# Kernel optimization log

Measured on AMD Instinct MI355X. Metric: run time of the kernel, lower is better.

The kernel has to match this reference:

```python
import math
import jax, jax.numpy as jnp
from jax import lax
import numpy as np

SIGMA_SCALES = [0.6 * 2 ** i for i in range(6)]  # [0.6, 1.2, 2.4, 4.8, 9.6, 19.2]


def _gauss1d(sigma: float, ks: int) -> np.ndarray:
    # ax = arange(-ks//2+1, ks//2+1) for odd ks == arange(ks) - ks//2 (symmetric)
    ax = np.arange(ks, dtype=np.float32) - ks // 2
    k = np.exp(-(ax ** 2) / (2.0 * sigma ** 2))
    return (k / k.sum()).astype(np.float32)


def _kernel_size(sigma: float) -> int:
    return max(7, 2 * math.ceil(3.0 * sigma) + 1)


def _gaussian_blur(img, sigma):
    # Separable depthwise Gaussian: the torch module's 2D kernel
    # exp(-(x^2+y^2)/2s^2)/Z factors exactly into outer(g1, g1) of normalized 1D kernels.
    B, C, H, W = img.shape
    ks = _kernel_size(sigma)
    p = ks // 2
    g1 = jnp.asarray(_gauss1d(sigma, ks), dtype=img.dtype)
    x = jnp.pad(img, ((0, 0), (0, 0), (p, p), (p, p)), mode='reflect')
    kh = jnp.broadcast_to(g1.reshape(1, 1, ks, 1), (C, 1, ks, 1))
    kw = jnp.broadcast_to(g1.reshape(1, 1, 1, ks), (C, 1, 1, ks))
    dn = ('NCHW', 'OIHW', 'NCHW')
    x = lax.conv_general_dilated(x, kh, (1, 1), 'VALID', dimension_numbers=dn,
                                 feature_group_count=C)
    x = lax.conv_general_dilated(x, kw, (1, 1), 'VALID', dimension_numbers=dn,
                                 feature_group_count=C)
    return x  # (B, C, H, W)


def setup_inputs() -> dict:
    key = jax.random.key(0)
    img = jax.random.normal(key, (8, 3, 512, 512), dtype=jnp.float32)
    return {"img": img}


def reference(img) -> jnp.ndarray:
    # gaussians = [img, G(s0)*img, G(s1)*img, ...]; each scale filters the ORIGINAL img.
    gaussians = [img]
    for sigma in SIGMA_SCALES:
        gaussians.append(_gaussian_blur(img, sigma))
    n = len(gaussians)
    subbands = [gaussians[i + 1] - gaussians[i] for i in range(n - 1)]
    subbands.append(gaussians[-1])
    return jnp.stack(subbands, axis=1)  # (B, len(scales)+1, C, H, W)
```

## Files before the change

### kernel.cpp

```cpp
#include <hip/hip_runtime.h>
#include <cmath>
#include <cstddef>

#define BATCH 8
#define CH    3
#define HH    512
#define WW    512
#define NSLOT 7
#define HWX   (HH*WW)

__device__ __host__ __forceinline__ int refl(int i, int n) {
    i = i < 0 ? -i : i;
    return i >= n ? 2 * n - 2 - i : i;
}

constexpr double cexp_(double x) {
    double r = x / 64.0, term = 1.0, s = 1.0;
    for (int i = 1; i < 26; ++i) { term *= r / i; s += term; }
    for (int j = 0; j < 6; ++j) s *= s;
    return s;
}

template<int KS> struct WArr { float w[KS + 16]; };

template<int KS>
constexpr WArr<KS> make_w(double sg) {
    WArr<KS> a{};
    double tmp[KS] = {};
    double sum = 0.0;
    for (int t = 0; t < KS; ++t) {
        const double ax = (double)(t - KS / 2);
        tmp[t] = cexp_(-(ax * ax) / (2.0 * sg * sg));
        sum += tmp[t];
    }
    for (int i = 0; i < KS + 16; ++i) a.w[i] = 0.0f;
    for (int t = 0; t < KS; ++t) a.w[8 + t] = (float)(tmp[t] / sum);
    return a;
}

__device__ constexpr WArr<7>   CW0 = make_w<7>(0.6);
__device__ constexpr WArr<9>   CW1 = make_w<9>(1.2);
__device__ constexpr WArr<17>  CW2 = make_w<17>(2.4);
__device__ constexpr WArr<31>  CW3 = make_w<31>(4.8);
__device__ constexpr WArr<59>  CW4 = make_w<59>(9.6);
__device__ constexpr WArr<117> CW5 = make_w<117>(19.2);

template<int KS> struct VWArr {
    static constexpr int TPAD = (KS + 30) & ~15;
    float w[TPAD + 16];
};

template<int KS>
constexpr VWArr<KS> make_vw(double sg) {
    VWArr<KS> a{};
    double tmp[KS] = {};
    double sum = 0.0;
    for (int t = 0; t < KS; ++t) {
        const double ax = (double)(t - KS / 2);
        tmp[t] = cexp_(-(ax * ax) / (2.0 * sg * sg));
        sum += tmp[t];
    }
    for (int i = 0; i < VWArr<KS>::TPAD + 16; ++i) a.w[i] = 0.0f;
    for (int t = 0; t < KS; ++t) a.w[16 + t] = (float)(tmp[t] / sum);
    return a;
}

__device__ constexpr VWArr<7>   VW0 = make_vw<7>(0.6);
__device__ constexpr VWArr<9>   VW1 = make_vw<9>(1.2);
__device__ constexpr VWArr<17>  VW2 = make_vw<17>(2.4);
__device__ constexpr VWArr<31>  VW3 = make_vw<31>(4.8);
__device__ constexpr VWArr<59>  VW4 = make_vw<59>(9.6);
__device__ constexpr VWArr<117> VW5 = make_vw<117>(19.2);

template<int KS, int PD>
__device__ __forceinline__ void vpass16(const float4* __restrict__ img4,
                                        float4* __restrict__ dst,
                                        int xt, int y0, const float* __restrict__ vw)
{
    constexpr int TPAD = (KS + 30) & ~15;
    float4 acc[16];
#pragma unroll
    for (int j = 0; j < 16; ++j) acc[j] = make_float4(0.f, 0.f, 0.f, 0.f);

    float ww[16];
#pragma unroll
    for (int m = 0; m < 16; ++m) ww[m] = vw[m];

#pragma unroll 1
    for (int tb = 0; tb < TPAD; tb += 16) {
        float wn[16];
#pragma unroll
        for (int k = 0; k < 16; ++k) wn[k] = vw[tb + 16 + k];
#pragma unroll
        for (int k = 0; k < 16; ++k) {
            const int yi = refl(y0 - PD + tb + k, HH);
            const float4 v = img4[(size_t)yi * (WW / 4) + xt];
#pragma unroll
            for (int j = 0; j < 16; ++j) {
                const int mi = 16 + k - j;
                const float wt = (mi < 16) ? ww[mi] : wn[mi - 16];
                acc[j].x = fmaf(wt, v.x, acc[j].x);
                acc[j].y = fmaf(wt, v.y, acc[j].y);
                acc[j].z = fmaf(wt, v.z, acc[j].z);
                acc[j].w = fmaf(wt, v.w, acc[j].w);
            }
        }
#pragma unroll
        for (int m = 0; m < 16; ++m) ww[m] = wn[m];
    }
#pragma unroll
    for (int j = 0; j < 16; ++j) dst[(size_t)(y0 + j) * (WW / 4) + xt] = acc[j];
}

__global__ __launch_bounds__(128) void vpass6_kernel(const float* __restrict__ img,
                                                     float* __restrict__ out)
{
    const int s  = blockIdx.x;
    const int xt = threadIdx.x;
    const int y0 = blockIdx.y * 16;
    const int bc = blockIdx.z;
    const int b = bc / CH, c = bc - b * CH;
    const float4* img4 = (const float4*)img + (size_t)bc * (HWX / 4);
    float4* dst = (float4*)out + ((size_t)((b * NSLOT + s + 1) * CH) + c) * (HWX / 4);
    switch (s) {
        case 0: vpass16<  7,  3>(img4, dst, xt, y0, VW0.w); break;
        case 1: vpass16<  9,  4>(img4, dst, xt, y0, VW1.w); break;
        case 2: vpass16< 17,  8>(img4, dst, xt, y0, VW2.w); break;
        case 3: vpass16< 31, 15>(img4, dst, xt, y0, VW3.w); break;
        case 4: vpass16< 59, 29>(img4, dst, xt, y0, VW4.w); break;
        default:vpass16<117, 58>(img4, dst, xt, y0, VW5.w); break;
    }
}

template<int KS>
__device__ __forceinline__ float4 hblur4c(const float* __restrict__ lrow, int xt,
                                          const WArr<KS>& W)
{
    constexpr int NT = (KS + 3) & ~3;
    const float4* l4 = (const float4*)lrow;
    float cb[16];
    {
        float4 t0 = l4[xt + 0];
        cb[0] = t0.x; cb[1] = t0.y; cb[2] = t0.z; cb[3] = t0.w;
        float4 t1 = l4[xt + 1];
        cb[4] = t1.x; cb[5] = t1.y; cb[6] = t1.z; cb[7] = t1.w;
    }
    float a[4] = {0.f, 0.f, 0.f, 0.f};
#pragma unroll
    for (int tb = 0; tb < NT; tb += 4) {
        const int ls = ((tb >> 2) + 2) & 3;
        float4 tn = l4[xt + (tb >> 2) + 2];
        cb[ls * 4 + 0] = tn.x; cb[ls * 4 + 1] = tn.y;
        cb[ls * 4 + 2] = tn.z; cb[ls * 4 + 3] = tn.w;
#pragma unroll
        for (int tt = 0; tt < 4; ++tt) {
            const float wt = W.w[8 + tb + tt];
#pragma unroll
            for (int j = 0; j < 4; ++j) {
                const int q    = tt + j;
                const int slot = ((tb >> 2) + (q >> 2)) & 3;
                a[j] = fmaf(wt, cb[slot * 4 + (q & 3)], a[j]);
            }
        }
    }
    return make_float4(a[0], a[1], a[2], a[3]);
}

#define LDSROW 3348

template<int OFF, int LEN, int PD>
__device__ __forceinline__ void stage_row(float* __restrict__ L,
                                          const float* __restrict__ g, int xt)
{
    const float4 v = ((const float4*)g)[xt];
    if constexpr ((PD & 3) == 0) {
        ((float4*)(L + OFF + PD))[xt] = v;
    } else {
        float* d = L + OFF + PD + 4 * xt;
        d[0] = v.x; d[1] = v.y; d[2] = v.z; d[3] = v.w;
    }
    if (xt < PD) L[OFF + xt] = g[PD - xt];
    for (int i = PD + 512 + xt; i < LEN; i += 128)
        L[OFF + i] = g[2 * WW - 2 - (i - PD)];
}

__device__ __forceinline__ float4 f4sub(float4 a, float4 b) {
    return make_float4(a.x - b.x, a.y - b.y, a.z - b.z, a.w - b.w);
}

__global__ __launch_bounds__(256) void hdiff6_kernel(const float* __restrict__ img,
                                                     float* __restrict__ out)
{
    __shared__ __align__(16) float lds[2][LDSROW];
    const int xt = threadIdx.x;
    const int r  = threadIdx.y;
    const int y  = blockIdx.y * 2 + r;
    const int bc = blockIdx.z;
    const int b = bc / CH, c = bc - b * CH;
    float* L = lds[r];

    const size_t rowoff = (size_t)y * WW;
    constexpr size_t SSTR = (size_t)CH * HWX;
    const float* g1 = out + ((size_t)((b * NSLOT + 1) * CH) + c) * HWX + rowoff;
    stage_row<   0, 524,  3>(L, g1,            xt);
    stage_row< 524, 528,  4>(L, g1 + 1 * SSTR, xt);
    stage_row<1052, 536,  8>(L, g1 + 2 * SSTR, xt);
    stage_row<1588, 548, 15>(L, g1 + 3 * SSTR, xt);
    stage_row<2136, 576, 29>(L, g1 + 4 * SSTR, xt);
    stage_row<2712, 636, 58>(L, g1 + 5 * SSTR, xt);
    __syncthreads();

    float4* out4 = (float4*)out;
    const size_t pbase = (size_t)y * (WW / 4) + xt;
#define OSL(s) (out4 + ((size_t)((b * NSLOT + (s)) * CH) + c) * (HWX / 4) + pbase)

    float4 gp = ((const float4*)(img + (size_t)bc * HWX + rowoff))[xt];
    float4 g;
    g = hblur4c<  7>(L +    0, xt, CW0); *OSL(0) = f4sub(g, gp); gp = g;
    g = hblur4c<  9>(L +  524, xt, CW1); *OSL(1) = f4sub(g, gp); gp = g;
    g = hblur4c< 17>(L + 1052, xt, CW2); *OSL(2) = f4sub(g, gp); gp = g;
    g = hblur4c< 31>(L + 1588, xt, CW3); *OSL(3) = f4sub(g, gp); gp = g;
    g = hblur4c< 59>(L + 2136, xt, CW4); *OSL(4) = f4sub(g, gp); gp = g;
    g = hblur4c<117>(L + 2712, xt, CW5); *OSL(5) = f4sub(g, gp);
    *OSL(6) = g;
#undef OSL
}

extern "C" void kernel_launch(void* const* d_in, const int* in_sizes, int n_in,
                              void* d_out, int out_size, void* d_ws, size_t ws_size,
                              hipStream_t stream) {
    const float* img = (const float*)d_in[0];
    float* out = (float*)d_out;

    const dim3 bv(128, 1), gv(6, HH / 16, BATCH * CH);
    hipLaunchKernelGGL(vpass6_kernel, gv, bv, 0, stream, img, out);

    const dim3 bh(128, 2), gh(1, HH / 2, BATCH * CH);
    hipLaunchKernelGGL(hdiff6_kernel, gh, bh, 0, stream, img, out);
}
```

Measured before the change: 381.4 us.

## Remap blocks so each XCD owns whole images; align horizontal LDS rows

Both kernels now use a flat 1D grid and decode the block index so that consecutive blocks round-robin across the 8 XCDs while each XCD keeps the same batch-channel planes. The goal is for each XCD's L2 to hold its own image planes and intermediate rows. The horizontal kernel drops to one row per 128-thread block, and the blur kernels are zero-padded on the left so every LDS row offset is 16-byte aligned and can be staged with float4 stores. The horizontal blur adds a 6-slot register window with a deeper prefetch and loads the img row before staging. The cost is a few extra zero-weight FMAs per tap group and the loss of two-row blocks.

After: 366.9 us. 1.04x faster.

```diff
diff --git a/kernel.cpp b/kernel.cpp
--- a/kernel.cpp
+++ b/kernel.cpp
@@ -21,11 +21,11 @@
     return s;
 }
 
-template<int KS> struct WArr { float w[KS + 16]; };
-
-template<int KS>
-constexpr WArr<KS> make_w(double sg) {
-    WArr<KS> a{};
+template<int KSE> struct WArr { float w[KSE + 16]; };
+
+template<int KSE, int KS>
+constexpr WArr<KSE> make_wz(double sg) {
+    WArr<KSE> a{};
     double tmp[KS] = {};
     double sum = 0.0;
     for (int t = 0; t < KS; ++t) {
@@ -33,17 +33,18 @@
         tmp[t] = cexp_(-(ax * ax) / (2.0 * sg * sg));
         sum += tmp[t];
     }
-    for (int i = 0; i < KS + 16; ++i) a.w[i] = 0.0f;
-    for (int t = 0; t < KS; ++t) a.w[8 + t] = (float)(tmp[t] / sum);
+    for (int i = 0; i < KSE + 16; ++i) a.w[i] = 0.0f;
+    constexpr int Z = KSE - KS;
+    for (int t = 0; t < KS; ++t) a.w[8 + Z + t] = (float)(tmp[t] / sum);
     return a;
 }
 
-__device__ constexpr WArr<7>   CW0 = make_w<7>(0.6);
-__device__ constexpr WArr<9>   CW1 = make_w<9>(1.2);
-__device__ constexpr WArr<17>  CW2 = make_w<17>(2.4);
-__device__ constexpr WArr<31>  CW3 = make_w<31>(4.8);
-__device__ constexpr WArr<59>  CW4 = make_w<59>(9.6);
-__device__ constexpr WArr<117> CW5 = make_w<117>(19.2);
+__device__ constexpr WArr<8>   CW0 = make_wz<8,   7>(0.6);
+__device__ constexpr WArr<9>   CW1 = make_wz<9,   9>(1.2);
+__device__ constexpr WArr<17>  CW2 = make_wz<17, 17>(2.4);
+__device__ constexpr WArr<32>  CW3 = make_wz<32, 31>(4.8);
+__device__ constexpr WArr<62>  CW4 = make_wz<62, 59>(9.6);
+__device__ constexpr WArr<119> CW5 = make_wz<119,117>(19.2);
 
 template<int KS> struct VWArr {
     static constexpr int TPAD = (KS + 30) & ~15;
@@ -115,10 +116,15 @@
 __global__ __launch_bounds__(128) void vpass6_kernel(const float* __restrict__ img,
                                                      float* __restrict__ out)
 {
-    const int s  = blockIdx.x;
-    const int xt = threadIdx.x;
-    const int y0 = blockIdx.y * 16;
-    const int bc = blockIdx.z;
+    const int n   = blockIdx.x;
+    const int xcd = n & 7;
+    const int k   = n >> 3;
+    const int bcg = k / 192;
+    const int rem = k - bcg * 192;
+    const int s   = rem >> 5;
+    const int y0  = (rem & 31) << 4;
+    const int bc  = bcg * 8 + xcd;
+    const int xt  = threadIdx.x;
     const int b = bc / CH, c = bc - b * CH;
     const float4* img4 = (const float4*)img + (size_t)bc * (HWX / 4);
     float4* dst = (float4*)out + ((size_t)((b * NSLOT + s + 1) * CH) + c) * (HWX / 4);
@@ -132,33 +138,37 @@
     }
 }
 
-template<int KS>
-__device__ __forceinline__ float4 hblur4c(const float* __restrict__ lrow, int xt,
-                                          const WArr<KS>& W)
-{
-    constexpr int NT = (KS + 3) & ~3;
+template<int KSE>
+__device__ __forceinline__ float4 hblur6(const float* __restrict__ lrow, int xt,
+                                         const WArr<KSE>& W)
+{
+    constexpr int NT = (KSE + 3) & ~3;
+    constexpr int G  = NT / 4;
+    constexpr int NR = G + 2;
     const float4* l4 = (const float4*)lrow;
-    float cb[16];
-    {
-        float4 t0 = l4[xt + 0];
-        cb[0] = t0.x; cb[1] = t0.y; cb[2] = t0.z; cb[3] = t0.w;
-        float4 t1 = l4[xt + 1];
-        cb[4] = t1.x; cb[5] = t1.y; cb[6] = t1.z; cb[7] = t1.w;
+    float cb[24];
+#pragma unroll
+    for (int s = 0; s < (NR < 4 ? NR : 4); ++s) {
+        const float4 t = l4[xt + s];
+        cb[(s % 6) * 4 + 0] = t.x; cb[(s % 6) * 4 + 1] = t.y;
+        cb[(s % 6) * 4 + 2] = t.z; cb[(s % 6) * 4 + 3] = t.w;
     }
     float a[4] = {0.f, 0.f, 0.f, 0.f};
 #pragma unroll
-    for (int tb = 0; tb < NT; tb += 4) {
-        const int ls = ((tb >> 2) + 2) & 3;
-        float4 tn = l4[xt + (tb >> 2) + 2];
-        cb[ls * 4 + 0] = tn.x; cb[ls * 4 + 1] = tn.y;
-        cb[ls * 4 + 2] = tn.z; cb[ls * 4 + 3] = tn.w;
+    for (int g = 0; g < G; ++g) {
+        if (g + 4 < NR) {
+            const int sl = (g + 4) % 6;
+            const float4 t = l4[xt + g + 4];
+            cb[sl * 4 + 0] = t.x; cb[sl * 4 + 1] = t.y;
+            cb[sl * 4 + 2] = t.z; cb[sl * 4 + 3] = t.w;
+        }
 #pragma unroll
         for (int tt = 0; tt < 4; ++tt) {
-            const float wt = W.w[8 + tb + tt];
+            const float wt = W.w[8 + 4 * g + tt];
 #pragma unroll
             for (int j = 0; j < 4; ++j) {
                 const int q    = tt + j;
-                const int slot = ((tb >> 2) + (q >> 2)) & 3;
+                const int slot = (g + (q >> 2)) % 6;
                 a[j] = fmaf(wt, cb[slot * 4 + (q & 3)], a[j]);
             }
         }
@@ -166,62 +176,60 @@
     return make_float4(a[0], a[1], a[2], a[3]);
 }
 
-#define LDSROW 3348
-
-template<int OFF, int LEN, int PD>
+#define LDSROW 3352
+
+template<int OFF, int LEN, int PDA>
 __device__ __forceinline__ void stage_row(float* __restrict__ L,
                                           const float* __restrict__ g, int xt)
 {
-    const float4 v = ((const float4*)g)[xt];
-    if constexpr ((PD & 3) == 0) {
-        ((float4*)(L + OFF + PD))[xt] = v;
-    } else {
-        float* d = L + OFF + PD + 4 * xt;
-        d[0] = v.x; d[1] = v.y; d[2] = v.z; d[3] = v.w;
-    }
-    if (xt < PD) L[OFF + xt] = g[PD - xt];
-    for (int i = PD + 512 + xt; i < LEN; i += 128)
-        L[OFF + i] = g[2 * WW - 2 - (i - PD)];
+    ((float4*)(L + OFF + PDA))[xt] = ((const float4*)g)[xt];
+    if (xt < PDA) L[OFF + xt] = g[PDA - xt];
+    for (int i = PDA + 512 + xt; i < LEN; i += 128)
+        L[OFF + i] = g[1022 - (i - PDA)];
 }
 
 __device__ __forceinline__ float4 f4sub(float4 a, float4 b) {
     return make_float4(a.x - b.x, a.y - b.y, a.z - b.z, a.w - b.w);
 }
 
-__global__ __launch_bounds__(256) void hdiff6_kernel(const float* __restrict__ img,
+__global__ __launch_bounds__(128) void hdiff6_kernel(const float* __restrict__ img,
                                                      float* __restrict__ out)
 {
-    __shared__ __align__(16) float lds[2][LDSROW];
-    const int xt = threadIdx.x;
-    const int r  = threadIdx.y;
-    const int y  = blockIdx.y * 2 + r;
-    const int bc = blockIdx.z;
+    __shared__ __align__(16) float L[LDSROW];
+    const int n   = blockIdx.x;
+    const int xcd = n & 7;
+    const int k   = n >> 3;
+    const int bcg = k >> 9;
+    const int y   = k & 511;
+    const int bc  = bcg * 8 + xcd;
+    const int xt  = threadIdx.x;
     const int b = bc / CH, c = bc - b * CH;
-    float* L = lds[r];
 
     const size_t rowoff = (size_t)y * WW;
+    const float4 gp0 = ((const float4*)(img + (size_t)bc * HWX + rowoff))[xt];
+
     constexpr size_t SSTR = (size_t)CH * HWX;
     const float* g1 = out + ((size_t)((b * NSLOT + 1) * CH) + c) * HWX + rowoff;
-    stage_row<   0, 524,  3>(L, g1,            xt);
+    stage_row<   0, 524,  4>(L, g1,            xt);
     stage_row< 524, 528,  4>(L, g1 + 1 * SSTR, xt);
     stage_row<1052, 536,  8>(L, g1 + 2 * SSTR, xt);
-    stage_row<1588, 548, 15>(L, g1 + 3 * SSTR, xt);
-    stage_row<2136, 576, 29>(L, g1 + 4 * SSTR, xt);
-    stage_row<2712, 636, 58>(L, g1 + 5 * SSTR, xt);
+    stage_row<1588, 548, 16>(L, g1 + 3 * SSTR, xt);
+    stage_row<2136, 580, 32>(L, g1 + 4 * SSTR, xt);
+    stage_row<2716, 636, 60>(L, g1 + 5 * SSTR, xt);
     __syncthreads();
 
     float4* out4 = (float4*)out;
     const size_t pbase = (size_t)y * (WW / 4) + xt;
 #define OSL(s) (out4 + ((size_t)((b * NSLOT + (s)) * CH) + c) * (HWX / 4) + pbase)
 
-    float4 gp = ((const float4*)(img + (size_t)bc * HWX + rowoff))[xt];
+    float4 gp = gp0;
     float4 g;
-    g = hblur4c<  7>(L +    0, xt, CW0); *OSL(0) = f4sub(g, gp); gp = g;
-    g = hblur4c<  9>(L +  524, xt, CW1); *OSL(1) = f4sub(g, gp); gp = g;
-    g = hblur4c< 17>(L + 1052, xt, CW2); *OSL(2) = f4sub(g, gp); gp = g;
-    g = hblur4c< 31>(L + 1588, xt, CW3); *OSL(3) = f4sub(g, gp); gp = g;
-    g = hblur4c< 59>(L + 2136, xt, CW4); *OSL(4) = f4sub(g, gp); gp = g;
-    g = hblur4c<117>(L + 2712, xt, CW5); *OSL(5) = f4sub(g, gp);
+    g = hblur6<  8>(L +    0, xt, CW0); *OSL(0) = f4sub(g, gp); gp = g;
+    g = hblur6<  9>(L +  524, xt, CW1); *OSL(1) = f4sub(g, gp); gp = g;
+    g = hblur6< 17>(L + 1052, xt, CW2); *OSL(2) = f4sub(g, gp); gp = g;
+    g = hblur6< 32>(L + 1588, xt, CW3); *OSL(3) = f4sub(g, gp); gp = g;
+    g = hblur6< 62>(L + 2136, xt, CW4); *OSL(4) = f4sub(g, gp); gp = g;
+    g = hblur6<119>(L + 2716, xt, CW5); *OSL(5) = f4sub(g, gp);
     *OSL(6) = g;
 #undef OSL
 }
@@ -232,9 +240,7 @@
     const float* img = (const float*)d_in[0];
     float* out = (float*)d_out;
 
-    const dim3 bv(128, 1), gv(6, HH / 16, BATCH * CH);
-    hipLaunchKernelGGL(vpass6_kernel, gv, bv, 0, stream, img, out);
-
-    const dim3 bh(128, 2), gh(1, HH / 2, BATCH * CH);
-    hipLaunchKernelGGL(hdiff6_kernel, gh, bh, 0, stream, img, out);
-}
+    hipLaunchKernelGGL(vpass6_kernel, dim3(4608), dim3(128), 0, stream, img, out);
+
+    hipLaunchKernelGGL(hdiff6_kernel, dim3(12288), dim3(128), 0, stream, img, out);
+}
```
